# Optimization experiments

Measured on AMD Instinct MI355X. Metric: run time of the kernel, lower is better.

Reference implementation:

```python
import jax, jax.numpy as jnp
import numpy as np

N, E = 50000, 800000
D_IN, D_H, D_OUT = 128, 128, 64


def _gcn_conv(h, src, dst, norm, b, n):
    # h already linearly transformed: aggregate norm-weighted messages to dst
    msg = h[src] * norm[:, None]                      # [E+N, d]
    out = jax.ops.segment_sum(msg, dst, num_segments=n)
    return out + b


def setup_inputs() -> dict:
    key = jax.random.key(0)
    ks = jax.random.split(key, 5)
    x = jax.random.normal(ks[0], (N, D_IN), jnp.float32)
    edge_index = jax.random.randint(ks[1], (2, E), 0, N, jnp.int32)
    s1 = 1.0 / np.sqrt(D_IN)
    s2 = 1.0 / np.sqrt(D_H)
    W1 = jax.random.uniform(ks[2], (D_IN, D_H), jnp.float32, -s1, s1)
    b1 = jnp.zeros((D_H,), jnp.float32)
    W2 = jax.random.uniform(ks[3], (D_H, D_OUT), jnp.float32, -s2, s2)
    b2 = jnp.zeros((D_OUT,), jnp.float32)
    return {"x": x, "edge_index": edge_index, "W1": W1, "b1": b1, "W2": W2, "b2": b2}


def reference(x, edge_index, W1, b1, W2, b2):
    n = x.shape[0]
    loops = jnp.arange(n, dtype=edge_index.dtype)
    src = jnp.concatenate([edge_index[0], loops])     # add self-loops
    dst = jnp.concatenate([edge_index[1], loops])
    # symmetric normalization D^{-1/2} (A+I) D^{-1/2}; deg is in-degree incl. self-loop
    deg = jax.ops.segment_sum(jnp.ones(dst.shape[0], x.dtype), dst, num_segments=n)
    dinv = jnp.where(deg > 0, jax.lax.rsqrt(deg), 0.0)
    norm = dinv[src] * dinv[dst]
    h = _gcn_conv(x @ W1, src, dst, norm, b1, n)
    h = jax.nn.relu(h)                                # dropout = identity (eval)
    out = _gcn_conv(h @ W2, src, dst, norm, b2, n)
    return out
```

## Files before the change

### kernel.cpp

```cpp
#include <hip/hip_runtime.h>

typedef __bf16 bf16x8 __attribute__((ext_vector_type(8)));
typedef __bf16 bf16x4 __attribute__((ext_vector_type(4)));
typedef float  f32x4  __attribute__((ext_vector_type(4)));
typedef unsigned long long u64;

constexpr int PAD       = 64;
constexpr int BIN_SHIFT = 8;
constexpr int NBMAX     = 256;
constexpr int CAP       = 6144;
constexpr int SUBS      = 2;
constexpr int NPS       = 128;
constexpr int STR       = 68;
constexpr int CUR_STR   = 16;
constexpr int EPB       = 2048;
constexpr int GGN       = 32;


__global__ void init_k(int* __restrict__ bincur, __bf16* __restrict__ h1zero,
                       __bf16* __restrict__ h3zero) {
  int t = threadIdx.x;
  for (int i = t; i < NBMAX * CUR_STR; i += 256) bincur[i] = 0;
  if (t < 128) h1zero[t] = (__bf16)0.f;
  if (t < 64)  h3zero[t] = (__bf16)0.f;
}


__global__ __launch_bounds__(256) void bin_fill_k(
    const int* __restrict__ src, const int* __restrict__ dst,
    int* __restrict__ bincur, u64* __restrict__ bin_data, int E, int n) {
  __shared__ int hist[NBMAX];
  __shared__ int gbase[NBMAX];

  const int t = threadIdx.x;
  hist[t] = 0;
  __syncthreads();

  int base_e = blockIdx.x * EPB + t * 8;
  int m = E - base_e;
  m = m < 0 ? 0 : (m > 8 ? 8 : m);

  int sa[8], da[8], ba[8], ra[8];
  if (m == 8) {
    int4 s0 = *reinterpret_cast<const int4*>(src + base_e);
    int4 s1 = *reinterpret_cast<const int4*>(src + base_e + 4);
    int4 d0 = *reinterpret_cast<const int4*>(dst + base_e);
    int4 d1 = *reinterpret_cast<const int4*>(dst + base_e + 4);
    sa[0]=s0.x; sa[1]=s0.y; sa[2]=s0.z; sa[3]=s0.w;
    sa[4]=s1.x; sa[5]=s1.y; sa[6]=s1.z; sa[7]=s1.w;
    da[0]=d0.x; da[1]=d0.y; da[2]=d0.z; da[3]=d0.w;
    da[4]=d1.x; da[5]=d1.y; da[6]=d1.z; da[7]=d1.w;
  } else {
    for (int k = 0; k < m; ++k) { sa[k] = src[base_e + k]; da[k] = dst[base_e + k]; }
  }
  for (int k = 0; k < m; ++k) {
    ba[k] = da[k] >> BIN_SHIFT;
    ra[k] = atomicAdd(&hist[ba[k]], 1);
  }
  __syncthreads();

  if (hist[t] > 0) gbase[t] = atomicAdd(&bincur[t * CUR_STR], hist[t]);
  __syncthreads();

  for (int k = 0; k < m; ++k) {
    int pos = gbase[ba[k]] + ra[k];
    if (pos < CAP)
      bin_data[(size_t)ba[k] * CAP + pos] = ((u64)(unsigned)sa[k] << 32) | (unsigned)da[k];
  }
}


__global__ __launch_bounds__(256) void gemm1_k(const float* __restrict__ X,
                                               const float* __restrict__ W,
                                               __bf16* __restrict__ C, int n) {
  constexpr int K = 128, KP = 136, NC = 128, NT = 8, KC = 4;
  __shared__ __bf16 WT[NC * KP];

  const int t = threadIdx.x;
  for (int idx = t; idx < K * NC / 4; idx += 256) {
    int col = idx & 127;
    int k4  = idx >> 7;
    bf16x4 w;
    w[0] = (__bf16)W[(k4 * 4 + 0) * NC + col];
    w[1] = (__bf16)W[(k4 * 4 + 1) * NC + col];
    w[2] = (__bf16)W[(k4 * 4 + 2) * NC + col];
    w[3] = (__bf16)W[(k4 * 4 + 3) * NC + col];
    *reinterpret_cast<bf16x4*>(&WT[col * KP + k4 * 4]) = w;
  }
  __syncthreads();

  const int lane = t & 63;
  const int lr = lane & 15;
  const int lg = lane >> 4;

  bf16x8 bfrag[NT][KC];
#pragma unroll
  for (int nt = 0; nt < NT; ++nt)
#pragma unroll
    for (int kc = 0; kc < KC; ++kc)
      bfrag[nt][kc] = *reinterpret_cast<const bf16x8*>(
          &WT[(nt * 16 + lr) * KP + kc * 32 + lg * 8]);

  const int gw = blockIdx.x * 4 + (t >> 6);
  const int nw = gridDim.x * 4;
  const int mtiles = (n + 15) / 16;

  for (int mt = gw; mt < mtiles; mt += nw) {
    const int row  = mt * 16 + lr;
    const int crow = (row < n) ? row : (n - 1);

    bf16x8 afrag[KC];
#pragma unroll
    for (int kc = 0; kc < KC; ++kc) {
      const f32x4* p = reinterpret_cast<const f32x4*>(
          X + (size_t)crow * K + kc * 32 + lg * 8);
      f32x4 v0 = p[0], v1 = p[1];
      bf16x8 a;
      a[0] = (__bf16)v0[0]; a[1] = (__bf16)v0[1];
      a[2] = (__bf16)v0[2]; a[3] = (__bf16)v0[3];
      a[4] = (__bf16)v1[0]; a[5] = (__bf16)v1[1];
      a[6] = (__bf16)v1[2]; a[7] = (__bf16)v1[3];
      afrag[kc] = a;
    }

    f32x4 acc[NT];
#pragma unroll
    for (int nt = 0; nt < NT; ++nt) acc[nt] = (f32x4){0.f, 0.f, 0.f, 0.f};
#pragma unroll
    for (int kc = 0; kc < KC; ++kc)
#pragma unroll
      for (int nt = 0; nt < NT; ++nt)
        acc[nt] = __builtin_amdgcn_mfma_f32_16x16x32_bf16(afrag[kc], bfrag[nt][kc],
                                                          acc[nt], 0, 0, 0);

#pragma unroll
    for (int nt = 0; nt < NT; ++nt)
#pragma unroll
      for (int r = 0; r < 4; ++r) {
        int orow = mt * 16 + lg * 4 + r;
        if (orow < n) C[(size_t)orow * NC + nt * 16 + lr] = (__bf16)acc[nt][r];
      }
  }
}


__global__ __launch_bounds__(512) void csr_build_k(const int* __restrict__ bincur,
                                                   const u64* __restrict__ bin_data,
                                                   int* __restrict__ srcs_pad,
                                                   int* __restrict__ cnt,
                                                   float* __restrict__ dinv,
                                                   __bf16* __restrict__ h1b, int n) {
  __shared__ int rows[NPS * STR];
  __shared__ int lcnt[NPS];

  const int bin = blockIdx.x / SUBS;
  const int sub = blockIdx.x % SUBS;
  const int lo  = (bin << BIN_SHIFT) + sub * NPS;
  const int hi  = min(n, lo + NPS);

  for (int i = threadIdx.x; i < NPS * STR; i += 512) rows[i] = n;
  for (int i = threadIdx.x; i < NPS; i += 512) lcnt[i] = 0;
  __syncthreads();

  int cntE = bincur[bin * CUR_STR];
  cntE = cntE < CAP ? cntE : CAP;
  const u64* bd = bin_data + (size_t)bin * CAP;

  for (int i = threadIdx.x; i < cntE; i += 512) {
    u64 p = bd[i];
    int d = (int)(p & 0xffffffffu);
    unsigned l = (unsigned)(d - lo);
    if (l < (unsigned)NPS) {
      int q = atomicAdd(&lcnt[l], 1);
      if (q < PAD) rows[l * STR + q] = (int)(p >> 32);
    }
  }
  __syncthreads();

  for (int i = threadIdx.x; i < NPS * (PAD / 4); i += 512) {
    int nl = i >> 4;
    int c4 = i & 15;
    int g = lo + nl;
    if (g < hi)
      *reinterpret_cast<int4*>(&srcs_pad[(size_t)g * PAD + c4 * 4]) =
          *reinterpret_cast<const int4*>(&rows[nl * STR + c4 * 4]);
  }
  for (int i = threadIdx.x; i < NPS; i += 512) {
    int g = lo + i;
    if (g < hi) {
      int c = lcnt[i];
      cnt[g] = c;
      dinv[g] = rsqrtf((float)(c + 1));
    }
  }
  bf16x8* h8 = reinterpret_cast<bf16x8*>(h1b);
  for (int i = threadIdx.x; i < NPS * 16; i += 512) {
    int nl = i >> 4;
    int c8 = i & 15;
    int g = lo + nl;
    if (g < hi) {
      float di = rsqrtf((float)(lcnt[nl] + 1));
      bf16x8 v = h8[(size_t)g * 16 + c8];
      bf16x8 o;
#pragma unroll
      for (int q = 0; q < 8; ++q) o[q] = (__bf16)((float)v[q] * di);
      h8[(size_t)g * 16 + c8] = o;
    }
  }
}


__global__ __launch_bounds__(256) void gather_gemm2_k(
    const __bf16* __restrict__ h1b, const int* __restrict__ cnt,
    const int* __restrict__ srcs_pad, const float* __restrict__ dinv,
    const float* __restrict__ b1, const float* __restrict__ W2,
    __bf16* __restrict__ h3b, int n) {
  constexpr int K  = 128;
  constexpr int KP = 136;
  constexpr int KC = 4;

  __shared__ __bf16 W2T[64 * KP];
  __shared__ __bf16 aggT[GGN * KP];

  const int t = threadIdx.x;

  for (int idx = t; idx < K * 64 / 4; idx += 256) {
    int col = idx & 63;
    int k4  = idx >> 6;
    bf16x4 w;
    w[0] = (__bf16)W2[(k4 * 4 + 0) * 64 + col];
    w[1] = (__bf16)W2[(k4 * 4 + 1) * 64 + col];
    w[2] = (__bf16)W2[(k4 * 4 + 2) * 64 + col];
    w[3] = (__bf16)W2[(k4 * 4 + 3) * 64 + col];
    *reinterpret_cast<bf16x4*>(&W2T[col * KP + k4 * 4]) = w;
  }

  const int base = blockIdx.x * GGN;
  const bf16x8* h8 = reinterpret_cast<const bf16x8*>(h1b);
#pragma unroll
  for (int pass = 0; pass < 2; ++pass) {
    const int nl = pass * 16 + (t >> 4);
    const int d8 = t & 15;
    const int node = base + nl;
    bf16x8 ov;
    if (node < n) {
      int c = cnt[node];
      c = c < PAD ? c : PAD;
      const float di = dinv[node];
      const int* row = srcs_pad + (size_t)node * PAD;
      bf16x8 sv = h8[(size_t)node * 16 + d8];

      float acc[8];
#pragma unroll
      for (int q = 0; q < 8; ++q) acc[q] = 0.f;

      for (int j0 = 0; j0 < c; j0 += 8) {
        int4 a = *reinterpret_cast<const int4*>(row + j0);
        int4 b = *reinterpret_cast<const int4*>(row + j0 + 4);
        bf16x8 v0 = h8[(size_t)a.x * 16 + d8];
        bf16x8 v1 = h8[(size_t)a.y * 16 + d8];
        bf16x8 v2 = h8[(size_t)a.z * 16 + d8];
        bf16x8 v3 = h8[(size_t)a.w * 16 + d8];
        bf16x8 v4 = h8[(size_t)b.x * 16 + d8];
        bf16x8 v5 = h8[(size_t)b.y * 16 + d8];
        bf16x8 v6 = h8[(size_t)b.z * 16 + d8];
        bf16x8 v7 = h8[(size_t)b.w * 16 + d8];
#pragma unroll
        for (int q = 0; q < 8; ++q)
          acc[q] += ((float)v0[q] + (float)v1[q]) + ((float)v2[q] + (float)v3[q]) +
                    ((float)v4[q] + (float)v5[q]) + ((float)v6[q] + (float)v7[q]);
      }
#pragma unroll
      for (int q = 0; q < 8; ++q) {
        float val = (acc[q] + (float)sv[q]) * di + b1[d8 * 8 + q];
        ov[q] = (__bf16)fmaxf(val, 0.f);
      }
    } else {
#pragma unroll
      for (int q = 0; q < 8; ++q) ov[q] = (__bf16)0.f;
    }
    *reinterpret_cast<bf16x8*>(&aggT[nl * KP + d8 * 8]) = ov;
  }
  __syncthreads();

  const int lane = t & 63;
  const int lr = lane & 15;
  const int lg = lane >> 4;
  const int wv = t >> 6;
  const int mrow = (wv & 1) * 16;
  const int ch   = wv >> 1;

  bf16x8 bfrag[2][KC];
#pragma unroll
  for (int nt = 0; nt < 2; ++nt)
#pragma unroll
    for (int kc = 0; kc < KC; ++kc)
      bfrag[nt][kc] = *reinterpret_cast<const bf16x8*>(
          &W2T[((ch * 2 + nt) * 16 + lr) * KP + kc * 32 + lg * 8]);

  bf16x8 afrag[KC];
#pragma unroll
  for (int kc = 0; kc < KC; ++kc)
    afrag[kc] = *reinterpret_cast<const bf16x8*>(
        &aggT[(mrow + lr) * KP + kc * 32 + lg * 8]);

  f32x4 acc[2];
#pragma unroll
  for (int nt = 0; nt < 2; ++nt) acc[nt] = (f32x4){0.f, 0.f, 0.f, 0.f};
#pragma unroll
  for (int kc = 0; kc < KC; ++kc)
#pragma unroll
    for (int nt = 0; nt < 2; ++nt)
      acc[nt] = __builtin_amdgcn_mfma_f32_16x16x32_bf16(afrag[kc], bfrag[nt][kc],
                                                        acc[nt], 0, 0, 0);

#pragma unroll
  for (int r = 0; r < 4; ++r) {
    int orow = base + mrow + lg * 4 + r;
    if (orow < n) {
      float sc = dinv[orow];
#pragma unroll
      for (int nt = 0; nt < 2; ++nt)
        h3b[(size_t)orow * 64 + (ch * 2 + nt) * 16 + lr] = (__bf16)(acc[nt][r] * sc);
    }
  }
}


template<int D, bool RELU_OUT, bool OUT_BF16>
__global__ __launch_bounds__(256) void gather_bf_k(const __bf16* __restrict__ h,
                                                   const int* __restrict__ cnt,
                                                   const int* __restrict__ srcs_pad,
                                                   const float* __restrict__ dinv,
                                                   const float* __restrict__ bias,
                                                   void* __restrict__ outv, int n) {
  constexpr int L = D / 8;
  int t = blockIdx.x * 256 + threadIdx.x;
  int node = t / L;
  int d8 = t % L;
  if (node >= n) return;

  int c = cnt[node];
  c = c < PAD ? c : PAD;
  const float di = dinv[node];
  const int* row = srcs_pad + (size_t)node * PAD;
  const bf16x8* h8 = reinterpret_cast<const bf16x8*>(h);
  bf16x8 sv = h8[(size_t)node * L + d8];

  float acc[8];
#pragma unroll
  for (int q = 0; q < 8; ++q) acc[q] = 0.f;

  for (int j0 = 0; j0 < c; j0 += 8) {
    int4 a = *reinterpret_cast<const int4*>(row + j0);
    int4 b = *reinterpret_cast<const int4*>(row + j0 + 4);
    bf16x8 v0 = h8[(size_t)a.x * L + d8];
    bf16x8 v1 = h8[(size_t)a.y * L + d8];
    bf16x8 v2 = h8[(size_t)a.z * L + d8];
    bf16x8 v3 = h8[(size_t)a.w * L + d8];
    bf16x8 v4 = h8[(size_t)b.x * L + d8];
    bf16x8 v5 = h8[(size_t)b.y * L + d8];
    bf16x8 v6 = h8[(size_t)b.z * L + d8];
    bf16x8 v7 = h8[(size_t)b.w * L + d8];
#pragma unroll
    for (int q = 0; q < 8; ++q)
      acc[q] += ((float)v0[q] + (float)v1[q]) + ((float)v2[q] + (float)v3[q]) +
                ((float)v4[q] + (float)v5[q]) + ((float)v6[q] + (float)v7[q]);
  }

  float o[8];
#pragma unroll
  for (int q = 0; q < 8; ++q) {
    float b = bias[d8 * 8 + q];
    float val = (acc[q] + (float)sv[q]) * di + b;
    o[q] = RELU_OUT ? fmaxf(val, 0.f) : val;
  }

  if (OUT_BF16) {
    bf16x8 ov;
#pragma unroll
    for (int q = 0; q < 8; ++q) ov[q] = (__bf16)o[q];
    reinterpret_cast<bf16x8*>(outv)[(size_t)node * L + d8] = ov;
  } else {
    f32x4 lo = {o[0], o[1], o[2], o[3]};
    f32x4 hi = {o[4], o[5], o[6], o[7]};
    f32x4* op = reinterpret_cast<f32x4*>((float*)outv + (size_t)node * D + d8 * 8);
    op[0] = lo;
    op[1] = hi;
  }
}


extern "C" void kernel_launch(void* const* d_in, const int* in_sizes, int n_in,
                              void* d_out, int out_size, void* d_ws, size_t ws_size,
                              hipStream_t stream) {
  const float* x  = (const float*)d_in[0];
  const int*   ei = (const int*)d_in[1];
  const float* W1 = (const float*)d_in[2];
  const float* b1 = (const float*)d_in[3];
  const float* W2 = (const float*)d_in[4];
  const float* b2 = (const float*)d_in[5];

  const int n = in_sizes[0] / 128;
  const int E = in_sizes[1] / 2;
  const int* src = ei;
  const int* dst = ei + E;
  float* out = (float*)d_out;

  const int NBIN = (n + ((1 << BIN_SHIFT) - 1)) >> BIN_SHIFT;

  int*   bincur   = (int*)d_ws;
  int*   cnt      = (int*)d_ws + NBMAX * CUR_STR;
  float* dinv     = (float*)d_ws + NBMAX * CUR_STR + n;
  int*   srcs_pad = (int*)d_ws + NBMAX * CUR_STR + 2 * n;
  size_t w = (size_t)NBMAX * CUR_STR + 2 * n + (size_t)n * PAD;
  __bf16* h1b     = (__bf16*)((int*)d_ws + w);   w += (size_t)(n + 1) * 64;
  __bf16* scratch = (__bf16*)((int*)d_ws + w);   w += (size_t)n * 64;
  __bf16* h3b     = (__bf16*)((int*)d_ws + w);
  u64* bin_data = (u64*)scratch;

  init_k<<<1, 256, 0, stream>>>(bincur, h1b + (size_t)n * 128, h3b + (size_t)n * 64);

  const int fillB = (E + EPB - 1) / EPB;
  bin_fill_k<<<fillB, 256, 0, stream>>>(src, dst, bincur, bin_data, E, n);

  gemm1_k<<<256, 256, 0, stream>>>(x, W1, h1b, n);

  csr_build_k<<<NBIN * SUBS, 512, 0, stream>>>(bincur, bin_data, srcs_pad, cnt, dinv, h1b, n);

  gather_gemm2_k<<<(n + GGN - 1) / GGN, 256, 0, stream>>>(
      h1b, cnt, srcs_pad, dinv, b1, W2, h3b, n);

  {
    long long t = (long long)n * 8;
    gather_bf_k<64, false, false><<<(int)((t + 255) / 256), 256, 0, stream>>>(
        h3b, cnt, srcs_pad, dinv, b2, out, n);
  }
}
```

Baseline: 103.0 us.

## Fuse edge binning and first GEMM into one heterogeneous launch

Merges the edge bin-fill kernel and the X·W1 GEMM into a single launch. The first blocks do binning and the remaining blocks do the GEMM, so the two independent stages run concurrently and one launch is saved. Each GEMM block now handles one 64-column half of W1, which shrinks shared memory and B-fragment registers and may raise occupancy. The cost is that each X row tile is read and converted twice, once per column half.

```diff
diff --git a/kernel.cpp b/kernel.cpp
--- a/kernel.cpp
+++ b/kernel.cpp
@@ -26,65 +26,70 @@
 }
 
 
-__global__ __launch_bounds__(256) void bin_fill_k(
+__global__ __launch_bounds__(256) void fused_fill_gemm_k(
     const int* __restrict__ src, const int* __restrict__ dst,
-    int* __restrict__ bincur, u64* __restrict__ bin_data, int E, int n) {
-  __shared__ int hist[NBMAX];
-  __shared__ int gbase[NBMAX];
+    int* __restrict__ bincur, u64* __restrict__ bin_data, int E, int fillB,
+    const float* __restrict__ X, const float* __restrict__ W,
+    __bf16* __restrict__ C, int n) {
+  constexpr int K = 128, KP = 136, NC = 128, NT = 4, KC = 4;
+
+  __shared__ __align__(16) char smem[64 * KP * 2];
 
   const int t = threadIdx.x;
-  hist[t] = 0;
-  __syncthreads();
-
-  int base_e = blockIdx.x * EPB + t * 8;
-  int m = E - base_e;
-  m = m < 0 ? 0 : (m > 8 ? 8 : m);
-
-  int sa[8], da[8], ba[8], ra[8];
-  if (m == 8) {
-    int4 s0 = *reinterpret_cast<const int4*>(src + base_e);
-    int4 s1 = *reinterpret_cast<const int4*>(src + base_e + 4);
-    int4 d0 = *reinterpret_cast<const int4*>(dst + base_e);
-    int4 d1 = *reinterpret_cast<const int4*>(dst + base_e + 4);
-    sa[0]=s0.x; sa[1]=s0.y; sa[2]=s0.z; sa[3]=s0.w;
-    sa[4]=s1.x; sa[5]=s1.y; sa[6]=s1.z; sa[7]=s1.w;
-    da[0]=d0.x; da[1]=d0.y; da[2]=d0.z; da[3]=d0.w;
-    da[4]=d1.x; da[5]=d1.y; da[6]=d1.z; da[7]=d1.w;
-  } else {
-    for (int k = 0; k < m; ++k) { sa[k] = src[base_e + k]; da[k] = dst[base_e + k]; }
-  }
-  for (int k = 0; k < m; ++k) {
-    ba[k] = da[k] >> BIN_SHIFT;
-    ra[k] = atomicAdd(&hist[ba[k]], 1);
-  }
-  __syncthreads();
-
-  if (hist[t] > 0) gbase[t] = atomicAdd(&bincur[t * CUR_STR], hist[t]);
-  __syncthreads();
-
-  for (int k = 0; k < m; ++k) {
-    int pos = gbase[ba[k]] + ra[k];
-    if (pos < CAP)
-      bin_data[(size_t)ba[k] * CAP + pos] = ((u64)(unsigned)sa[k] << 32) | (unsigned)da[k];
-  }
-}
-
-
-__global__ __launch_bounds__(256) void gemm1_k(const float* __restrict__ X,
-                                               const float* __restrict__ W,
-                                               __bf16* __restrict__ C, int n) {
-  constexpr int K = 128, KP = 136, NC = 128, NT = 8, KC = 4;
-  __shared__ __bf16 WT[NC * KP];
-
-  const int t = threadIdx.x;
-  for (int idx = t; idx < K * NC / 4; idx += 256) {
-    int col = idx & 127;
-    int k4  = idx >> 7;
+
+  if ((int)blockIdx.x < fillB) {
+    int* hist  = (int*)smem;
+    int* gbase = (int*)(smem + 1024);
+
+    hist[t] = 0;
+    __syncthreads();
+
+    int base_e = blockIdx.x * EPB + t * 8;
+    int m = E - base_e;
+    m = m < 0 ? 0 : (m > 8 ? 8 : m);
+
+    int sa[8], da[8], ba[8], ra[8];
+    if (m == 8) {
+      int4 s0 = *reinterpret_cast<const int4*>(src + base_e);
+      int4 s1 = *reinterpret_cast<const int4*>(src + base_e + 4);
+      int4 d0 = *reinterpret_cast<const int4*>(dst + base_e);
+      int4 d1 = *reinterpret_cast<const int4*>(dst + base_e + 4);
+      sa[0]=s0.x; sa[1]=s0.y; sa[2]=s0.z; sa[3]=s0.w;
+      sa[4]=s1.x; sa[5]=s1.y; sa[6]=s1.z; sa[7]=s1.w;
+      da[0]=d0.x; da[1]=d0.y; da[2]=d0.z; da[3]=d0.w;
+      da[4]=d1.x; da[5]=d1.y; da[6]=d1.z; da[7]=d1.w;
+    } else {
+      for (int k = 0; k < m; ++k) { sa[k] = src[base_e + k]; da[k] = dst[base_e + k]; }
+    }
+    for (int k = 0; k < m; ++k) {
+      ba[k] = da[k] >> BIN_SHIFT;
+      ra[k] = atomicAdd(&hist[ba[k]], 1);
+    }
+    __syncthreads();
+
+    if (hist[t] > 0) gbase[t] = atomicAdd(&bincur[t * CUR_STR], hist[t]);
+    __syncthreads();
+
+    for (int k = 0; k < m; ++k) {
+      int pos = gbase[ba[k]] + ra[k];
+      if (pos < CAP)
+        bin_data[(size_t)ba[k] * CAP + pos] = ((u64)(unsigned)sa[k] << 32) | (unsigned)da[k];
+    }
+    return;
+  }
+
+  const int gb = blockIdx.x - fillB;
+  const int ch = gb & 1;
+  __bf16* WT = (__bf16*)smem;
+
+  for (int idx = t; idx < K * 64 / 4; idx += 256) {
+    int col = idx & 63;
+    int k4  = idx >> 6;
     bf16x4 w;
-    w[0] = (__bf16)W[(k4 * 4 + 0) * NC + col];
-    w[1] = (__bf16)W[(k4 * 4 + 1) * NC + col];
-    w[2] = (__bf16)W[(k4 * 4 + 2) * NC + col];
-    w[3] = (__bf16)W[(k4 * 4 + 3) * NC + col];
+    w[0] = (__bf16)W[(k4 * 4 + 0) * NC + ch * 64 + col];
+    w[1] = (__bf16)W[(k4 * 4 + 1) * NC + ch * 64 + col];
+    w[2] = (__bf16)W[(k4 * 4 + 2) * NC + ch * 64 + col];
+    w[3] = (__bf16)W[(k4 * 4 + 3) * NC + ch * 64 + col];
     *reinterpret_cast<bf16x4*>(&WT[col * KP + k4 * 4]) = w;
   }
   __syncthreads();
@@ -101,8 +106,8 @@
       bfrag[nt][kc] = *reinterpret_cast<const bf16x8*>(
           &WT[(nt * 16 + lr) * KP + kc * 32 + lg * 8]);
 
-  const int gw = blockIdx.x * 4 + (t >> 6);
-  const int nw = gridDim.x * 4;
+  const int gw = (gb >> 1) * 4 + (t >> 6);
+  const int nw = ((gridDim.x - fillB) >> 1) * 4;
   const int mtiles = (n + 15) / 16;
 
   for (int mt = gw; mt < mtiles; mt += nw) {
@@ -138,7 +143,8 @@
 #pragma unroll
       for (int r = 0; r < 4; ++r) {
         int orow = mt * 16 + lg * 4 + r;
-        if (orow < n) C[(size_t)orow * NC + nt * 16 + lr] = (__bf16)acc[nt][r];
+        if (orow < n)
+          C[(size_t)orow * NC + ch * 64 + nt * 16 + lr] = (__bf16)acc[nt][r];
       }
   }
 }
@@ -422,9 +428,9 @@
   init_k<<<1, 256, 0, stream>>>(bincur, h1b + (size_t)n * 128, h3b + (size_t)n * 64);
 
   const int fillB = (E + EPB - 1) / EPB;
-  bin_fill_k<<<fillB, 256, 0, stream>>>(src, dst, bincur, bin_data, E, n);
-
-  gemm1_k<<<256, 256, 0, stream>>>(x, W1, h1b, n);
+  const int gemmB = 256;
+  fused_fill_gemm_k<<<fillB + gemmB, 256, 0, stream>>>(
+      src, dst, bincur, bin_data, E, fillB, x, W1, h1b, n);
 
   csr_build_k<<<NBIN * SUBS, 512, 0, stream>>>(bincur, bin_data, srcs_pad, cnt, dinv, h1b, n);
 
```

Result: faster. 98.26 us (-4.6%).
